# Kernel tuning notes

Measured on AMD Instinct MI355X. Metric: run time of the kernel, lower is better.

The kernel has to match this reference:

```python
import jax, jax.numpy as jnp
import numpy as np

N = 50000        # num_nodes
E = 1_600_000    # num_edges
C = 64           # out_channels
P = 10           # periods (window_size)


def _glorot(k, shape):
    lim = np.sqrt(6.0 / (shape[0] + shape[1]))
    return jax.random.uniform(k, shape, jnp.float32, -lim, lim)


def setup_inputs() -> dict:
    key = jax.random.key(0)
    ks = jax.random.split(key, 12)
    x = jax.random.normal(ks[0], (N, 1, P), jnp.float32)
    edge_index = jax.random.randint(ks[1], (2, E), 0, N, dtype=jnp.int64)
    inp = {
        "x": x,
        "edge_index": edge_index,
        # GCNConv weights/biases for the 3 gates (in_channels=1 -> C)
        "w_cz": _glorot(ks[2], (1, C)), "b_cz": jnp.zeros((C,), jnp.float32),
        "w_cr": _glorot(ks[3], (1, C)), "b_cr": jnp.zeros((C,), jnp.float32),
        "w_ch": _glorot(ks[4], (1, C)), "b_ch": jnp.zeros((C,), jnp.float32),
        # GRU gate linears: Linear(2C -> C), stored as [in, out]
        "w_lz": _glorot(ks[5], (2 * C, C)), "b_lz": jnp.zeros((C,), jnp.float32),
        "w_lr": _glorot(ks[6], (2 * C, C)), "b_lr": jnp.zeros((C,), jnp.float32),
        "w_lh": _glorot(ks[7], (2 * C, C)), "b_lh": jnp.zeros((C,), jnp.float32),
        # temporal attention logits over periods
        "attention": jax.random.uniform(ks[8], (P,), jnp.float32),
        # output head Linear(C -> 1)
        "w_out": _glorot(ks[9], (C, 1)), "b_out": jnp.zeros((1,), jnp.float32),
    }
    return inp


def reference(x, edge_index, w_cz, b_cz, w_cr, b_cr, w_ch, b_ch,
              w_lz, b_lz, w_lr, b_lr, w_lh, b_lh, attention, w_out, b_out):
    # --- GCN symmetric normalization with self-loops (computed once) ---
    row, col = edge_index[0], edge_index[1]
    loop = jnp.arange(N, dtype=row.dtype)
    row_f = jnp.concatenate([row, loop])
    col_f = jnp.concatenate([col, loop])
    ones = jnp.ones(E + N, jnp.float32)
    deg = jax.ops.segment_sum(ones, col_f, num_segments=N)
    dinv = jnp.where(deg > 0, jax.lax.rsqrt(deg), 0.0)
    norm = dinv[row_f] * dinv[col_f]                       # [E+N]

    def gcn(xt, W, b):
        # xt: [N,1] -> lin -> propagate D^-1/2 (A+I) D^-1/2 -> + bias
        h = xt @ W                                          # [N,C]
        msg = h[row_f] * norm[:, None]                      # [E+N,C]
        return jax.ops.segment_sum(msg, col_f, num_segments=N) + b

    probs = jax.nn.softmax(attention)                       # [P]
    xs = jnp.transpose(x, (2, 0, 1))                        # [P,N,1]

    def step(carry, inp):
        H, Hacc = carry
        xt, p = inp
        Z = jax.nn.sigmoid(jnp.concatenate([gcn(xt, w_cz, b_cz), H], 1) @ w_lz + b_lz)
        R = jax.nn.sigmoid(jnp.concatenate([gcn(xt, w_cr, b_cr), H], 1) @ w_lr + b_lr)
        Ht = jnp.tanh(jnp.concatenate([gcn(xt, w_ch, b_ch), H * R], 1) @ w_lh + b_lh)
        Hn = Z * H + (1.0 - Z) * Ht
        return (Hn, Hacc + p * Hn), None

    H0 = jnp.zeros((N, C), jnp.float32)
    (_, Hacc), _ = jax.lax.scan(step, (H0, H0), (xs, probs))

    out = jnp.maximum(Hacc, 0.0) @ w_out + b_out            # ReLU + Linear(C->1)
    return out.squeeze(-1)                                   # [N]
```

## Files before the change

### kernel.cpp

```cpp
#include <hip/hip_runtime.h>
#include <math.h>


#define PT 10
#define PS 12
#define CC 64
#define CAP 96

__global__ void k_zero(unsigned int* p, int n) {
  int i = blockIdx.x * 256 + threadIdx.x;
  if (i < n) p[i] = 0u;
}

__global__ void k_deg(const int* __restrict__ col, unsigned int* deg, int E) {
  int e = blockIdx.x * 256 + threadIdx.x;
  if (e < E) atomicAdd(&deg[col[e]], 1u);
}

__global__ void k_scan1(const unsigned int* __restrict__ deg, unsigned int* rowstart,
                        unsigned int* blocksum, int n) {
  __shared__ unsigned int tmp[256];
  int i = blockIdx.x * 256 + threadIdx.x;
  unsigned int v = (i < n) ? deg[i] : 0u;
  tmp[threadIdx.x] = v;
  __syncthreads();
  for (int off = 1; off < 256; off <<= 1) {
    unsigned int t = (threadIdx.x >= off) ? tmp[threadIdx.x - off] : 0u;
    __syncthreads();
    tmp[threadIdx.x] += t;
    __syncthreads();
  }
  if (i < n) rowstart[i] = tmp[threadIdx.x] - v;
  if (threadIdx.x == 255) blocksum[blockIdx.x] = tmp[255];
}

__global__ void k_scan2(unsigned int* bs, int nb) {
  __shared__ unsigned int tmp[256];
  unsigned int v = (threadIdx.x < nb) ? bs[threadIdx.x] : 0u;
  tmp[threadIdx.x] = v;
  __syncthreads();
  for (int off = 1; off < 256; off <<= 1) {
    unsigned int t = (threadIdx.x >= off) ? tmp[threadIdx.x - off] : 0u;
    __syncthreads();
    tmp[threadIdx.x] += t;
    __syncthreads();
  }
  if (threadIdx.x < nb) bs[threadIdx.x] = tmp[threadIdx.x] - v;
}

__global__ void k_scan3(unsigned int* rowstart, const unsigned int* __restrict__ bs,
                        unsigned int* cursor, int n) {
  int i = blockIdx.x * 256 + threadIdx.x;
  if (i < n) {
    unsigned int v = rowstart[i] + bs[blockIdx.x];
    rowstart[i] = v;
    cursor[i] = v;
  }
}

__global__ void k_dinv_y(const unsigned int* __restrict__ deg, const float* __restrict__ x,
                         float* __restrict__ dinv, float* __restrict__ y, int n) {
  int v = blockIdx.x * 256 + threadIdx.x;
  if (v >= n) return;
  float di = rsqrtf((float)(deg[v] + 1u));
  dinv[v] = di;
  float* yr = y + (size_t)v * PS;
  const float* xr = x + (size_t)v * PT;
#pragma unroll
  for (int t = 0; t < PT; ++t) yr[t] = di * xr[t];
  yr[10] = 0.0f;
  yr[11] = 0.0f;
}

__global__ void k_scatter(const int* __restrict__ row, const int* __restrict__ col,
                          unsigned int* cnt_or_cursor, unsigned int* __restrict__ csr,
                          int E, int cap) {
  int e = blockIdx.x * 256 + threadIdx.x;
  if (e >= E) return;
  int c = col[e];
  unsigned int slot = atomicAdd(&cnt_or_cursor[c], 1u);
  if (cap > 0) {
    if (slot < (unsigned int)cap) csr[(size_t)c * cap + slot] = (unsigned int)row[e];
  } else {
    csr[slot] = (unsigned int)row[e];
  }
}

__global__ __launch_bounds__(256) void k_gather(
    const unsigned int* __restrict__ csr, const unsigned int* __restrict__ starts,
    const unsigned int* __restrict__ counts, const float* __restrict__ y,
    const float* __restrict__ dinv, float* __restrict__ s, int n, int cap) {
  int tid = blockIdx.x * 256 + threadIdx.x;
  int v = tid >> 2, l = tid & 3;
  if (v >= n) return;
  unsigned int cnt = counts[v];
  unsigned int start;
  if (cap > 0) {
    start = (unsigned int)v * (unsigned int)cap;
    if (cnt > (unsigned int)cap) cnt = (unsigned int)cap;
  } else {
    start = starts[v];
  }
  float a[PS];
#pragma unroll
  for (int t = 0; t < PS; ++t) a[t] = 0.0f;
  unsigned int end = start + cnt;
  for (unsigned int e = start + (unsigned int)l; e < end; e += 4u) {
    unsigned int r = csr[e];
    const float4* yr = (const float4*)(y + (size_t)r * PS);
    float4 b0 = yr[0], b1 = yr[1], b2 = yr[2];
    a[0] += b0.x; a[1] += b0.y; a[2] += b0.z; a[3] += b0.w;
    a[4] += b1.x; a[5] += b1.y; a[6] += b1.z; a[7] += b1.w;
    a[8] += b2.x; a[9] += b2.y; a[10] += b2.z; a[11] += b2.w;
  }
#pragma unroll
  for (int m = 1; m < 4; m <<= 1) {
#pragma unroll
    for (int t = 0; t < PS; ++t) a[t] += __shfl_xor(a[t], m, 64);
  }
  if (l == 0) {
    float di = dinv[v];
    const float4* ys = (const float4*)(y + (size_t)v * PS);
    float4 b0 = ys[0], b1 = ys[1], b2 = ys[2];
    float4 o0, o1, o2;
    o0.x = di * (a[0] + b0.x); o0.y = di * (a[1] + b0.y);
    o0.z = di * (a[2] + b0.z); o0.w = di * (a[3] + b0.w);
    o1.x = di * (a[4] + b1.x); o1.y = di * (a[5] + b1.y);
    o1.z = di * (a[6] + b1.z); o1.w = di * (a[7] + b1.w);
    o2.x = di * (a[8] + b2.x); o2.y = di * (a[9] + b2.y);
    o2.z = di * (a[10] + b2.z); o2.w = di * (a[11] + b2.w);
    float4* sv = (float4*)(s + (size_t)v * PS);
    sv[0] = o0; sv[1] = o1; sv[2] = o2;
  }
}

__global__ void k_sinit_fb(const float* __restrict__ y, const float* __restrict__ dinv,
                           float* __restrict__ s, int n) {
  int v = blockIdx.x * 256 + threadIdx.x;
  if (v >= n) return;
  float di = dinv[v];
#pragma unroll
  for (int t = 0; t < PS; ++t) s[(size_t)v * PS + t] = di * y[(size_t)v * PS + t];
}

__global__ void k_edge_fb(const int* __restrict__ row, const int* __restrict__ col,
                          const float* __restrict__ dinv, const float* __restrict__ y,
                          float* __restrict__ s, int E) {
  int e = blockIdx.x * 256 + threadIdx.x;
  if (e >= E) return;
  int r = row[e], c = col[e];
  float dc = dinv[c];
  const float* yr = y + (size_t)r * PS;
  float* sc = s + (size_t)c * PS;
#pragma unroll
  for (int t = 0; t < PT; ++t) atomicAdd(&sc[t], dc * yr[t]);
}

__global__ void k_prep(const float* wcz, const float* bcz, const float* wcr, const float* bcr,
                       const float* wch, const float* bch,
                       const float* wlz, const float* blz, const float* wlr, const float* blr,
                       const float* wlh, const float* blh, float* coef) {
  int c = threadIdx.x;
  float az = 0, ar = 0, ah = 0, bz = 0, br = 0, bh = 0;
  for (int m = 0; m < CC; ++m) {
    float z = wlz[m * CC + c], r = wlr[m * CC + c], h = wlh[m * CC + c];
    az += wcz[m] * z;  ar += wcr[m] * r;  ah += wch[m] * h;
    bz += bcz[m] * z;  br += bcr[m] * r;  bh += bch[m] * h;
  }
  coef[0 * CC + c] = az;
  coef[1 * CC + c] = ar;
  coef[2 * CC + c] = ah;
  coef[3 * CC + c] = bz + blz[c];
  coef[4 * CC + c] = br + blr[c];
  coef[5 * CC + c] = bh + blh[c];
}

__device__ __forceinline__ float sigf(float v) { return 1.0f / (1.0f + __expf(-v)); }
__device__ __forceinline__ float tanhfastf(float v) { return 2.0f / (1.0f + __expf(-2.0f * v)) - 1.0f; }

__device__ __forceinline__ int swz(int r, int ch) { return (ch ^ ((r >> 2) & 7)) << 2; }

__global__ __launch_bounds__(256) void k_gru(
    const float* __restrict__ s, const float* __restrict__ coef,
    const float* __restrict__ wlz, const float* __restrict__ wlr, const float* __restrict__ wlh,
    const float* __restrict__ attention, const float* __restrict__ w_out,
    const float* __restrict__ b_out, float* __restrict__ out, int n) {
  __shared__ float HT[64][64];
  __shared__ float QT[64][64];
  __shared__ float ZB[64][64];
  __shared__ float sT[64][12];

  const int tid = threadIdx.x;
  const int i = tid >> 5;
  const int j = tid & 31;
  const int n0 = blockIdx.x * 64;

  for (int idx = tid; idx < 64 * 64; idx += 256) ((float*)HT)[idx] = 0.0f;
  for (int idx = tid; idx < 64 * PT; idx += 256) {
    int nn = idx / PT, t = idx - nn * PT;
    int g = n0 + nn;
    sT[nn][t] = (g < n) ? s[(size_t)g * PS + t] : 0.0f;
  }

  float att[PT];
#pragma unroll
  for (int t = 0; t < PT; ++t) att[t] = attention[t];
  float mx = att[0];
#pragma unroll
  for (int t = 1; t < PT; ++t) mx = fmaxf(mx, att[t]);
  float ssum = 0.0f;
#pragma unroll
  for (int t = 0; t < PT; ++t) { att[t] = __expf(att[t] - mx); ssum += att[t]; }
  float sinv = 1.0f / ssum;
#pragma unroll
  for (int t = 0; t < PT; ++t) att[t] *= sinv;

  const bool isZ = (j < 16);
  const int czr = isZ ? (4 * j) : (4 * (j - 16));
  const float4 aZR = *(const float4*)(coef + (isZ ? 0 : 64) + czr);
  const float4 bZR = *(const float4*)(coef + (isZ ? 192 : 256) + czr);
  const float* WZR = (isZ ? wlz : wlr) + 64 * CC + czr;
  const int c2 = 2 * j;
  const float2 aH = *(const float2*)(coef + 128 + c2);
  const float2 bH = *(const float2*)(coef + 320 + c2);
  const float* WH = wlh + 64 * CC + c2;
  const float2 wo2 = *(const float2*)(w_out + c2);

  float hacc[8][2];
#pragma unroll
  for (int nn = 0; nn < 8; ++nn) { hacc[nn][0] = 0.0f; hacc[nn][1] = 0.0f; }

  __syncthreads();

  for (int t = 0; t < PT; ++t) {
    float sloc[8];
#pragma unroll
    for (int nn = 0; nn < 8; ++nn) sloc[nn] = sT[8 * i + nn][t];

    float acc[8][4];
#pragma unroll
    for (int nn = 0; nn < 8; ++nn) {
      acc[nn][0] = fmaf(sloc[nn], aZR.x, bZR.x);
      acc[nn][1] = fmaf(sloc[nn], aZR.y, bZR.y);
      acc[nn][2] = fmaf(sloc[nn], aZR.z, bZR.z);
      acc[nn][3] = fmaf(sloc[nn], aZR.w, bZR.w);
    }
#pragma unroll 4
    for (int k = 0; k < 64; ++k) {
      const float4 wv = *(const float4*)(WZR + (k << 6));
      const float4 h0 = *(const float4*)&HT[k][swz(k, 2 * i)];
      const float4 h1 = *(const float4*)&HT[k][swz(k, 2 * i + 1)];
      const float hh[8] = {h0.x, h0.y, h0.z, h0.w, h1.x, h1.y, h1.z, h1.w};
      const float ww[4] = {wv.x, wv.y, wv.z, wv.w};
#pragma unroll
      for (int nn = 0; nn < 8; ++nn)
#pragma unroll
        for (int cc = 0; cc < 4; ++cc) acc[nn][cc] = fmaf(hh[nn], ww[cc], acc[nn][cc]);
    }

    if (isZ) {
#pragma unroll
      for (int cc = 0; cc < 4; ++cc) {
        int r = czr + cc;
        float4 z0, z1;
        z0.x = sigf(acc[0][cc]); z0.y = sigf(acc[1][cc]); z0.z = sigf(acc[2][cc]); z0.w = sigf(acc[3][cc]);
        z1.x = sigf(acc[4][cc]); z1.y = sigf(acc[5][cc]); z1.z = sigf(acc[6][cc]); z1.w = sigf(acc[7][cc]);
        *(float4*)&ZB[r][swz(r, 2 * i)] = z0;
        *(float4*)&ZB[r][swz(r, 2 * i + 1)] = z1;
      }
    } else {
#pragma unroll
      for (int cc = 0; cc < 4; ++cc) {
        int r = czr + cc;
        float4 h0 = *(const float4*)&HT[r][swz(r, 2 * i)];
        float4 h1 = *(const float4*)&HT[r][swz(r, 2 * i + 1)];
        float4 q0, q1;
        q0.x = h0.x * sigf(acc[0][cc]); q0.y = h0.y * sigf(acc[1][cc]);
        q0.z = h0.z * sigf(acc[2][cc]); q0.w = h0.w * sigf(acc[3][cc]);
        q1.x = h1.x * sigf(acc[4][cc]); q1.y = h1.y * sigf(acc[5][cc]);
        q1.z = h1.z * sigf(acc[6][cc]); q1.w = h1.w * sigf(acc[7][cc]);
        *(float4*)&QT[r][swz(r, 2 * i)] = q0;
        *(float4*)&QT[r][swz(r, 2 * i + 1)] = q1;
      }
    }
    __syncthreads();

    float acc2[8][2];
#pragma unroll
    for (int nn = 0; nn < 8; ++nn) {
      acc2[nn][0] = fmaf(sloc[nn], aH.x, bH.x);
      acc2[nn][1] = fmaf(sloc[nn], aH.y, bH.y);
    }
#pragma unroll 4
    for (int k = 0; k < 64; ++k) {
      const float2 wv = *(const float2*)(WH + (k << 6));
      const float4 q0 = *(const float4*)&QT[k][swz(k, 2 * i)];
      const float4 q1 = *(const float4*)&QT[k][swz(k, 2 * i + 1)];
      const float qq[8] = {q0.x, q0.y, q0.z, q0.w, q1.x, q1.y, q1.z, q1.w};
#pragma unroll
      for (int nn = 0; nn < 8; ++nn) {
        acc2[nn][0] = fmaf(qq[nn], wv.x, acc2[nn][0]);
        acc2[nn][1] = fmaf(qq[nn], wv.y, acc2[nn][1]);
      }
    }

    float hn[2][8];
#pragma unroll
    for (int cc = 0; cc < 2; ++cc) {
      int r = c2 + cc;
      float4 z0 = *(const float4*)&ZB[r][swz(r, 2 * i)];
      float4 z1 = *(const float4*)&ZB[r][swz(r, 2 * i + 1)];
      float4 h0 = *(const float4*)&HT[r][swz(r, 2 * i)];
      float4 h1 = *(const float4*)&HT[r][swz(r, 2 * i + 1)];
      const float zz[8] = {z0.x, z0.y, z0.z, z0.w, z1.x, z1.y, z1.z, z1.w};
      const float hh[8] = {h0.x, h0.y, h0.z, h0.w, h1.x, h1.y, h1.z, h1.w};
#pragma unroll
      for (int nn = 0; nn < 8; ++nn) {
        float ht = tanhfastf(acc2[nn][cc]);
        float v = zz[nn] * hh[nn] + (1.0f - zz[nn]) * ht;
        hn[cc][nn] = v;
        hacc[nn][cc] = fmaf(att[t], v, hacc[nn][cc]);
      }
    }
    __syncthreads();
#pragma unroll
    for (int cc = 0; cc < 2; ++cc) {
      int r = c2 + cc;
      float4 v0 = make_float4(hn[cc][0], hn[cc][1], hn[cc][2], hn[cc][3]);
      float4 v1 = make_float4(hn[cc][4], hn[cc][5], hn[cc][6], hn[cc][7]);
      *(float4*)&HT[r][swz(r, 2 * i)] = v0;
      *(float4*)&HT[r][swz(r, 2 * i + 1)] = v1;
    }
    __syncthreads();
  }

  float p[8];
#pragma unroll
  for (int nn = 0; nn < 8; ++nn)
    p[nn] = fmaxf(hacc[nn][0], 0.0f) * wo2.x + fmaxf(hacc[nn][1], 0.0f) * wo2.y;
#pragma unroll
  for (int m = 1; m < 32; m <<= 1) {
#pragma unroll
    for (int nn = 0; nn < 8; ++nn) p[nn] += __shfl_xor(p[nn], m, 64);
  }
  if (j == 0) {
    float bo = b_out[0];
#pragma unroll
    for (int nn = 0; nn < 8; ++nn) {
      int g = n0 + 8 * i + nn;
      if (g < n) out[g] = p[nn] + bo;
    }
  }
}

extern "C" void kernel_launch(void* const* d_in, const int* in_sizes, int n_in,
                              void* d_out, int out_size, void* d_ws, size_t ws_size,
                              hipStream_t stream) {
  const float* x    = (const float*)d_in[0];
  const int*   ei   = (const int*)d_in[1];
  const float* wcz  = (const float*)d_in[2];
  const float* bcz  = (const float*)d_in[3];
  const float* wcr  = (const float*)d_in[4];
  const float* bcr  = (const float*)d_in[5];
  const float* wch  = (const float*)d_in[6];
  const float* bch  = (const float*)d_in[7];
  const float* wlz  = (const float*)d_in[8];
  const float* blz  = (const float*)d_in[9];
  const float* wlr  = (const float*)d_in[10];
  const float* blr  = (const float*)d_in[11];
  const float* wlh  = (const float*)d_in[12];
  const float* blh  = (const float*)d_in[13];
  const float* att  = (const float*)d_in[14];
  const float* wout = (const float*)d_in[15];
  const float* bout = (const float*)d_in[16];
  float* out = (float*)d_out;

  const int N = out_size;
  const int E = in_sizes[1] / 2;
  const int* row = ei;
  const int* col = ei + E;

  char* ws = (char*)d_ws;
  size_t off = 0;
  auto alloc = [&](size_t bytes) {
    char* p = ws + off;
    off += (bytes + 15) & ~15ull;
    return p;
  };
  unsigned int* cnt  = (unsigned int*)alloc((size_t)N * 4);
  float*        dinv = (float*)alloc((size_t)N * 4);
  float*        y    = (float*)alloc((size_t)N * PS * 4);
  float*        s    = (float*)alloc((size_t)N * PS * 4);
  float*        coef = (float*)alloc(384 * 4);
  size_t commonEnd = off;

  const size_t needA = commonEnd + (size_t)N * CAP * 4;
  const size_t needB = commonEnd + (size_t)N * 8 + 256 * 4 + (size_t)E * 4 + 64;

  const int nbN = (N + 255) / 256;
  const int nbE = (E + 255) / 256;

  k_prep<<<1, 64, 0, stream>>>(wcz, bcz, wcr, bcr, wch, bch, wlz, blz, wlr, blr, wlh, blh, coef);

  if (ws_size >= needA) {
    unsigned int* csr = (unsigned int*)(ws + commonEnd);
    k_zero<<<nbN, 256, 0, stream>>>(cnt, N);
    k_scatter<<<nbE, 256, 0, stream>>>(row, col, cnt, csr, E, CAP);
    k_dinv_y<<<nbN, 256, 0, stream>>>(cnt, x, dinv, y, N);
    k_gather<<<(4 * N + 255) / 256, 256, 0, stream>>>(csr, nullptr, cnt, y, dinv, s, N, CAP);
  } else if (ws_size >= needB) {
    size_t o = commonEnd;
    unsigned int* rowstart = (unsigned int*)(ws + o); o += (size_t)N * 4;
    unsigned int* cursor   = (unsigned int*)(ws + o); o += (size_t)N * 4;
    unsigned int* blocksum = (unsigned int*)(ws + o); o += 256 * 4;
    unsigned int* csr      = (unsigned int*)(ws + o);
    k_zero<<<nbN, 256, 0, stream>>>(cnt, N);
    k_deg<<<nbE, 256, 0, stream>>>(col, cnt, E);
    k_scan1<<<nbN, 256, 0, stream>>>(cnt, rowstart, blocksum, N);
    k_scan2<<<1, 256, 0, stream>>>(blocksum, nbN);
    k_scan3<<<nbN, 256, 0, stream>>>(rowstart, blocksum, cursor, N);
    k_dinv_y<<<nbN, 256, 0, stream>>>(cnt, x, dinv, y, N);
    k_scatter<<<nbE, 256, 0, stream>>>(row, col, cursor, csr, E, 0);
    k_gather<<<(4 * N + 255) / 256, 256, 0, stream>>>(csr, rowstart, cnt, y, dinv, s, N, 0);
  } else {
    k_zero<<<nbN, 256, 0, stream>>>(cnt, N);
    k_deg<<<nbE, 256, 0, stream>>>(col, cnt, E);
    k_dinv_y<<<nbN, 256, 0, stream>>>(cnt, x, dinv, y, N);
    k_sinit_fb<<<nbN, 256, 0, stream>>>(y, dinv, s, N);
    k_edge_fb<<<nbE, 256, 0, stream>>>(row, col, dinv, y, s, E);
  }

  k_gru<<<(N + 63) / 64, 256, 0, stream>>>(s, coef, wlz, wlr, wlh, att, wout, bout, out, N);
}
```

Before: 573.3 us.

## Keep Z gate in registers, remove ZB buffer and one barrier per step

Each thread now computes both the Z and R gate pre-activations for the same two output channels it later updates, so the Z values and the old H values stay in registers instead of going through a shared ZB buffer. This drops one shared-memory array and one __syncthreads per timestep, because each thread overwrites only HT entries it alone reads. It also adds a min-blocks hint of 4 to launch_bounds. In exchange, R-gate work is no longer split across separate lanes, and register pressure rises from the held hold/zreg arrays under a tighter register cap.

```diff
diff --git a/kernel.cpp b/kernel.cpp
--- a/kernel.cpp
+++ b/kernel.cpp
@@ -180,14 +180,13 @@
 
 __device__ __forceinline__ int swz(int r, int ch) { return (ch ^ ((r >> 2) & 7)) << 2; }
 
-__global__ __launch_bounds__(256) void k_gru(
+__global__ __launch_bounds__(256, 4) void k_gru(
     const float* __restrict__ s, const float* __restrict__ coef,
     const float* __restrict__ wlz, const float* __restrict__ wlr, const float* __restrict__ wlh,
     const float* __restrict__ attention, const float* __restrict__ w_out,
     const float* __restrict__ b_out, float* __restrict__ out, int n) {
   __shared__ float HT[64][64];
   __shared__ float QT[64][64];
-  __shared__ float ZB[64][64];
   __shared__ float sT[64][12];
 
   const int tid = threadIdx.x;
@@ -215,14 +214,15 @@
 #pragma unroll
   for (int t = 0; t < PT; ++t) att[t] *= sinv;
 
-  const bool isZ = (j < 16);
-  const int czr = isZ ? (4 * j) : (4 * (j - 16));
-  const float4 aZR = *(const float4*)(coef + (isZ ? 0 : 64) + czr);
-  const float4 bZR = *(const float4*)(coef + (isZ ? 192 : 256) + czr);
-  const float* WZR = (isZ ? wlz : wlr) + 64 * CC + czr;
   const int c2 = 2 * j;
+  const float2 aZ = *(const float2*)(coef + 0 + c2);
+  const float2 aR = *(const float2*)(coef + 64 + c2);
   const float2 aH = *(const float2*)(coef + 128 + c2);
+  const float2 bZ = *(const float2*)(coef + 192 + c2);
+  const float2 bR = *(const float2*)(coef + 256 + c2);
   const float2 bH = *(const float2*)(coef + 320 + c2);
+  const float* WZ = wlz + 64 * CC + c2;
+  const float* WR = wlr + 64 * CC + c2;
   const float* WH = wlh + 64 * CC + c2;
   const float2 wo2 = *(const float2*)(w_out + c2);
 
@@ -240,48 +240,44 @@
     float acc[8][4];
 #pragma unroll
     for (int nn = 0; nn < 8; ++nn) {
-      acc[nn][0] = fmaf(sloc[nn], aZR.x, bZR.x);
-      acc[nn][1] = fmaf(sloc[nn], aZR.y, bZR.y);
-      acc[nn][2] = fmaf(sloc[nn], aZR.z, bZR.z);
-      acc[nn][3] = fmaf(sloc[nn], aZR.w, bZR.w);
+      acc[nn][0] = fmaf(sloc[nn], aZ.x, bZ.x);
+      acc[nn][1] = fmaf(sloc[nn], aZ.y, bZ.y);
+      acc[nn][2] = fmaf(sloc[nn], aR.x, bR.x);
+      acc[nn][3] = fmaf(sloc[nn], aR.y, bR.y);
     }
 #pragma unroll 4
     for (int k = 0; k < 64; ++k) {
-      const float4 wv = *(const float4*)(WZR + (k << 6));
+      const float2 wz = *(const float2*)(WZ + (k << 6));
+      const float2 wr = *(const float2*)(WR + (k << 6));
       const float4 h0 = *(const float4*)&HT[k][swz(k, 2 * i)];
       const float4 h1 = *(const float4*)&HT[k][swz(k, 2 * i + 1)];
       const float hh[8] = {h0.x, h0.y, h0.z, h0.w, h1.x, h1.y, h1.z, h1.w};
-      const float ww[4] = {wv.x, wv.y, wv.z, wv.w};
-#pragma unroll
-      for (int nn = 0; nn < 8; ++nn)
-#pragma unroll
-        for (int cc = 0; cc < 4; ++cc) acc[nn][cc] = fmaf(hh[nn], ww[cc], acc[nn][cc]);
-    }
-
-    if (isZ) {
-#pragma unroll
-      for (int cc = 0; cc < 4; ++cc) {
-        int r = czr + cc;
-        float4 z0, z1;
-        z0.x = sigf(acc[0][cc]); z0.y = sigf(acc[1][cc]); z0.z = sigf(acc[2][cc]); z0.w = sigf(acc[3][cc]);
-        z1.x = sigf(acc[4][cc]); z1.y = sigf(acc[5][cc]); z1.z = sigf(acc[6][cc]); z1.w = sigf(acc[7][cc]);
-        *(float4*)&ZB[r][swz(r, 2 * i)] = z0;
-        *(float4*)&ZB[r][swz(r, 2 * i + 1)] = z1;
+#pragma unroll
+      for (int nn = 0; nn < 8; ++nn) {
+        acc[nn][0] = fmaf(hh[nn], wz.x, acc[nn][0]);
+        acc[nn][1] = fmaf(hh[nn], wz.y, acc[nn][1]);
+        acc[nn][2] = fmaf(hh[nn], wr.x, acc[nn][2]);
+        acc[nn][3] = fmaf(hh[nn], wr.y, acc[nn][3]);
       }
-    } else {
-#pragma unroll
-      for (int cc = 0; cc < 4; ++cc) {
-        int r = czr + cc;
-        float4 h0 = *(const float4*)&HT[r][swz(r, 2 * i)];
-        float4 h1 = *(const float4*)&HT[r][swz(r, 2 * i + 1)];
-        float4 q0, q1;
-        q0.x = h0.x * sigf(acc[0][cc]); q0.y = h0.y * sigf(acc[1][cc]);
-        q0.z = h0.z * sigf(acc[2][cc]); q0.w = h0.w * sigf(acc[3][cc]);
-        q1.x = h1.x * sigf(acc[4][cc]); q1.y = h1.y * sigf(acc[5][cc]);
-        q1.z = h1.z * sigf(acc[6][cc]); q1.w = h1.w * sigf(acc[7][cc]);
-        *(float4*)&QT[r][swz(r, 2 * i)] = q0;
-        *(float4*)&QT[r][swz(r, 2 * i + 1)] = q1;
-      }
+    }
+
+    float hold[2][8], zreg[2][8];
+#pragma unroll
+    for (int cc = 0; cc < 2; ++cc) {
+      int r = c2 + cc;
+      float4 h0 = *(const float4*)&HT[r][swz(r, 2 * i)];
+      float4 h1 = *(const float4*)&HT[r][swz(r, 2 * i + 1)];
+      hold[cc][0] = h0.x; hold[cc][1] = h0.y; hold[cc][2] = h0.z; hold[cc][3] = h0.w;
+      hold[cc][4] = h1.x; hold[cc][5] = h1.y; hold[cc][6] = h1.z; hold[cc][7] = h1.w;
+      float4 q0, q1;
+      q0.x = hold[cc][0] * sigf(acc[0][2 + cc]); q0.y = hold[cc][1] * sigf(acc[1][2 + cc]);
+      q0.z = hold[cc][2] * sigf(acc[2][2 + cc]); q0.w = hold[cc][3] * sigf(acc[3][2 + cc]);
+      q1.x = hold[cc][4] * sigf(acc[4][2 + cc]); q1.y = hold[cc][5] * sigf(acc[5][2 + cc]);
+      q1.z = hold[cc][6] * sigf(acc[6][2 + cc]); q1.w = hold[cc][7] * sigf(acc[7][2 + cc]);
+      *(float4*)&QT[r][swz(r, 2 * i)] = q0;
+      *(float4*)&QT[r][swz(r, 2 * i + 1)] = q1;
+#pragma unroll
+      for (int nn = 0; nn < 8; ++nn) zreg[cc][nn] = sigf(acc[nn][cc]);
     }
     __syncthreads();
 
@@ -304,30 +300,20 @@
       }
     }
 
-    float hn[2][8];
 #pragma unroll
     for (int cc = 0; cc < 2; ++cc) {
       int r = c2 + cc;
-      float4 z0 = *(const float4*)&ZB[r][swz(r, 2 * i)];
-      float4 z1 = *(const float4*)&ZB[r][swz(r, 2 * i + 1)];
-      float4 h0 = *(const float4*)&HT[r][swz(r, 2 * i)];
-      float4 h1 = *(const float4*)&HT[r][swz(r, 2 * i + 1)];
-      const float zz[8] = {z0.x, z0.y, z0.z, z0.w, z1.x, z1.y, z1.z, z1.w};
-      const float hh[8] = {h0.x, h0.y, h0.z, h0.w, h1.x, h1.y, h1.z, h1.w};
+      float hn[8];
 #pragma unroll
       for (int nn = 0; nn < 8; ++nn) {
         float ht = tanhfastf(acc2[nn][cc]);
-        float v = zz[nn] * hh[nn] + (1.0f - zz[nn]) * ht;
-        hn[cc][nn] = v;
+        float z = zreg[cc][nn];
+        float v = z * hold[cc][nn] + (1.0f - z) * ht;
+        hn[nn] = v;
         hacc[nn][cc] = fmaf(att[t], v, hacc[nn][cc]);
       }
-    }
-    __syncthreads();
-#pragma unroll
-    for (int cc = 0; cc < 2; ++cc) {
-      int r = c2 + cc;
-      float4 v0 = make_float4(hn[cc][0], hn[cc][1], hn[cc][2], hn[cc][3]);
-      float4 v1 = make_float4(hn[cc][4], hn[cc][5], hn[cc][6], hn[cc][7]);
+      float4 v0 = make_float4(hn[0], hn[1], hn[2], hn[3]);
+      float4 v1 = make_float4(hn[4], hn[5], hn[6], hn[7]);
       *(float4*)&HT[r][swz(r, 2 * i)] = v0;
       *(float4*)&HT[r][swz(r, 2 * i + 1)] = v1;
     }
```

After: 551.5 us. 3.8% less time.
